# Performance work log

Hardware: AMD Instinct MI355X
Metric: run time of the kernel (lower is better)

Reference implementation:

```python
import jax, jax.numpy as jnp
import numpy as np

N = 100000      # nodes
E = 800000      # edges
IN = 256        # input feature dim
HID = 64        # hidden_channels (= per-head out_channels)
HEADS = 2       # num_heads
L = 2           # num_layers
C = 40          # class_num
ALPHA = 0.5
EPS = 1e-5


def setup_inputs() -> dict:
    key = jax.random.key(0)
    ks = jax.random.split(key, 14)
    s = 0.05
    inp = {
        "x": jax.random.normal(ks[0], (N, IN), dtype=jnp.float32),
        "edge_index": jax.random.randint(ks[1], (2, E), 0, N),
        "fc0_w": jax.random.normal(ks[2], (IN, HID), dtype=jnp.float32) * s,
        "fc0_b": jnp.zeros((HID,), jnp.float32),
        "ln_w": jnp.ones((L + 1, HID), jnp.float32),
        "ln_b": jnp.zeros((L + 1, HID), jnp.float32),
        "Wq": jax.random.normal(ks[3], (L, HID, HID * HEADS), dtype=jnp.float32) * s,
        "Wk": jax.random.normal(ks[4], (L, HID, HID * HEADS), dtype=jnp.float32) * s,
        "Wv": jax.random.normal(ks[5], (L, HID, HID * HEADS), dtype=jnp.float32) * s,
        "bq": jnp.zeros((L, HID * HEADS), jnp.float32),
        "bk": jnp.zeros((L, HID * HEADS), jnp.float32),
        "bv": jnp.zeros((L, HID * HEADS), jnp.float32),
        "fco_w": jax.random.normal(ks[6], (HID, C), dtype=jnp.float32) * s,
        "fco_b": jnp.zeros((C,), jnp.float32),
    }
    return inp


def _layernorm(x, w, b):
    mu = jnp.mean(x, axis=-1, keepdims=True)
    var = jnp.mean((x - mu) ** 2, axis=-1, keepdims=True)
    return (x - mu) * jax.lax.rsqrt(var + EPS) * w + b


def _simple_attn(q, k, v):
    # q,k: [N,H,M], v: [N,H,D]; kernelized (non-softmax) linear attention
    q = q / jnp.sqrt(jnp.sum(q * q))        # global L2 norm (torch.norm p=2)
    k = k / jnp.sqrt(jnp.sum(k * k))
    kvs = jnp.einsum('lhm,lhd->hmd', k, v)
    num = jnp.einsum('nhm,hmd->nhd', q, kvs) + jnp.sum(v, axis=0)  # [N,H,D]
    denom = jnp.einsum('nhm,hm->nh', q, jnp.sum(k, axis=0))[..., None]
    denom = denom + jnp.asarray(q.shape[0], q.dtype)
    return num / denom


def _gcn_conv(v, row, col):
    # v: [N,H,D]; out[n] = sum_{e: col[e]==n} w_e * v[row[e]]
    n = v.shape[0]
    deg = jax.ops.segment_sum(jnp.ones((row.shape[0],), v.dtype), col,
                              num_segments=n)
    val = jnp.sqrt(1.0 / deg[col]) * jnp.sqrt(1.0 / deg[row])
    val = jnp.nan_to_num(val, nan=0.0, posinf=0.0, neginf=0.0)
    v2 = v.reshape(n, -1)                    # [N, H*D]
    msg = val[:, None] * v2[row]             # [E, H*D]
    out = jax.ops.segment_sum(msg, col, num_segments=n)
    return out.reshape(v.shape)


def reference(x, edge_index, fc0_w, fc0_b, ln_w, ln_b, Wq, Wk, Wv, bq, bk, bv,
              fco_w, fco_b):
    row, col = edge_index[0], edge_index[1]
    h = x @ fc0_w + fc0_b
    h = _layernorm(h, ln_w[0], ln_b[0])
    h = jax.nn.relu(h)
    prev = h
    for i in range(L):
        q = (h @ Wq[i] + bq[i]).reshape(-1, HEADS, HID)
        k = (h @ Wk[i] + bk[i]).reshape(-1, HEADS, HID)
        v = (h @ Wv[i] + bv[i]).reshape(-1, HEADS, HID)
        out = _simple_attn(q, k, v) + _gcn_conv(v, row, col)
        out = out.mean(axis=1)               # mean over heads -> [N,HID]
        h = ALPHA * out + (1.0 - ALPHA) * prev
        h = _layernorm(h, ln_w[i + 1], ln_b[i + 1])
        prev = h
    return h @ fco_w + fco_b
```

## Files before the change

### kernel.cpp

```cpp
#include <hip/hip_runtime.h>
#include <math.h>

#define NNODES 100000
#define NEDGES 800000
#define DIN    256
#define HID    64
#define NC     40
#define NL     2
#define EPSL   1e-5f
#define CHUNK  1024
#define NCHUNK ((NNODES + CHUNK - 1) / CHUNK)
#define NB128  ((NNODES + 127) / 128)
#define NKVB   512
#define SLAB   8720

__device__ __forceinline__ float wave_allsum(float v) {
#pragma unroll
  for (int off = 32; off > 0; off >>= 1) v += __shfl_xor(v, off);
  return v;
}

__global__ void k_hist(const int* __restrict__ ei, int* __restrict__ deg) {
  for (int e = blockIdx.x * blockDim.x + threadIdx.x; e < NEDGES;
       e += gridDim.x * blockDim.x)
    atomicAdd(&deg[ei[NEDGES + e]], 1);
}

__global__ void k_scan1(const int* __restrict__ deg, int* __restrict__ csum) {
  __shared__ int sdata[256];
  int base = blockIdx.x * CHUNK;
  int s = 0;
  for (int t = threadIdx.x; t < CHUNK; t += 256) {
    int idx = base + t;
    if (idx < NNODES) s += deg[idx];
  }
  sdata[threadIdx.x] = s;
  __syncthreads();
  for (int off = 128; off > 0; off >>= 1) {
    if (threadIdx.x < off) sdata[threadIdx.x] += sdata[threadIdx.x + off];
    __syncthreads();
  }
  if (threadIdx.x == 0) csum[blockIdx.x] = sdata[0];
}

__global__ void k_scan2(const int* __restrict__ csum, int* __restrict__ cpref) {
  if (threadIdx.x == 0 && blockIdx.x == 0) {
    int run = 0;
    for (int i = 0; i < NCHUNK; ++i) { cpref[i] = run; run += csum[i]; }
  }
}

__global__ void k_scan3(const int* __restrict__ deg, const int* __restrict__ cpref,
                        int* __restrict__ offs) {
  __shared__ int bufA[CHUNK], bufB[CHUNK];
  int base = blockIdx.x * CHUNK;
  int orig[4];
#pragma unroll
  for (int i = 0; i < 4; ++i) {
    int t = threadIdx.x + i * 256;
    int idx = base + t;
    orig[i] = (idx < NNODES) ? deg[idx] : 0;
    bufA[t] = orig[i];
  }
  __syncthreads();
  int* src = bufA; int* dst = bufB;
  for (int off = 1; off < CHUNK; off <<= 1) {
#pragma unroll
    for (int i = 0; i < 4; ++i) {
      int t = threadIdx.x + i * 256;
      int vv = src[t];
      if (t >= off) vv += src[t - off];
      dst[t] = vv;
    }
    __syncthreads();
    int* tmp = src; src = dst; dst = tmp;
  }
  int cp = cpref[blockIdx.x];
#pragma unroll
  for (int i = 0; i < 4; ++i) {
    int t = threadIdx.x + i * 256;
    int idx = base + t;
    if (idx < NNODES) {
      offs[idx] = cp + src[t] - orig[i];
      if (idx == NNODES - 1) offs[NNODES] = cp + src[t];
    }
  }
}

__global__ void k_fill(const int* __restrict__ ei, const int* __restrict__ deg,
                       const int* __restrict__ offs, int* __restrict__ cursor,
                       int2* __restrict__ epack) {
  for (int e = blockIdx.x * blockDim.x + threadIdx.x; e < NEDGES;
       e += gridDim.x * blockDim.x) {
    int r = ei[e], c = ei[NEDGES + e];
    int pos = offs[c] + atomicAdd(&cursor[c], 1);
    int dc = deg[c], dr = deg[r];
    float w = (dr > 0)
        ? sqrtf(1.0f / (float)dc) * sqrtf(1.0f / (float)dr) : 0.0f;
    epack[pos] = make_int2(r, __float_as_int(w));
  }
}

__global__ __launch_bounds__(128) void k_fc0(
    const float* __restrict__ x, const float* __restrict__ w,
    const float* __restrict__ b, const float* __restrict__ lnw_,
    const float* __restrict__ lnb_, float* __restrict__ h) {
  __shared__ float xs[32 * 128];
  const int tid = threadIdx.x;
  const int base = blockIdx.x * 128;
  const int row = base + tid;
  const float4* x4 = (const float4*)x;
  float acc[64];
#pragma unroll
  for (int j = 0; j < 64; ++j) acc[j] = b[j];

  float4 pre[8];
#pragma unroll
  for (int i = 0; i < 8; ++i) {
    int r = i * 16 + (tid >> 3);
    int gr = base + r;
    pre[i] = (gr < NNODES) ? x4[(size_t)gr * 64 + (tid & 7)]
                           : make_float4(0.f, 0.f, 0.f, 0.f);
  }
  for (int c = 0; c < 8; ++c) {
    __syncthreads();
#pragma unroll
    for (int i = 0; i < 8; ++i) {
      int r = i * 16 + (tid >> 3);
      int kq = tid & 7;
      xs[(kq * 4 + 0) * 128 + r] = pre[i].x;
      xs[(kq * 4 + 1) * 128 + r] = pre[i].y;
      xs[(kq * 4 + 2) * 128 + r] = pre[i].z;
      xs[(kq * 4 + 3) * 128 + r] = pre[i].w;
    }
    __syncthreads();
    if (c < 7) {
#pragma unroll
      for (int i = 0; i < 8; ++i) {
        int r = i * 16 + (tid >> 3);
        int gr = base + r;
        pre[i] = (gr < NNODES) ? x4[(size_t)gr * 64 + (c + 1) * 8 + (tid & 7)]
                               : make_float4(0.f, 0.f, 0.f, 0.f);
      }
    }
    const float* wc = w + c * 32 * 64;
#pragma unroll 2
    for (int k = 0; k < 32; ++k) {
      float xv = xs[k * 128 + tid];
      const float* wr = wc + k * 64;
#pragma unroll
      for (int j = 0; j < 64; ++j) acc[j] = fmaf(xv, wr[j], acc[j]);
    }
  }
  if (row < NNODES) {
    float mu = 0.f;
#pragma unroll
    for (int j = 0; j < 64; ++j) mu += acc[j];
    mu *= (1.0f / 64.0f);
    float var = 0.f;
#pragma unroll
    for (int j = 0; j < 64; ++j) { float d = acc[j] - mu; var = fmaf(d, d, var); }
    float inv = 1.0f / sqrtf(var * (1.0f / 64.0f) + EPSL);
    float4* h4 = (float4*)(h + (size_t)row * 64);
#pragma unroll
    for (int jj = 0; jj < 16; ++jj) {
      float4 o;
      o.x = fmaxf((acc[4*jj+0] - mu) * inv * lnw_[4*jj+0] + lnb_[4*jj+0], 0.f);
      o.y = fmaxf((acc[4*jj+1] - mu) * inv * lnw_[4*jj+1] + lnb_[4*jj+1], 0.f);
      o.z = fmaxf((acc[4*jj+2] - mu) * inv * lnw_[4*jj+2] + lnb_[4*jj+2], 0.f);
      o.w = fmaxf((acc[4*jj+3] - mu) * inv * lnw_[4*jj+3] + lnb_[4*jj+3], 0.f);
      h4[jj] = o;
    }
  }
}

__global__ __launch_bounds__(128) void k_qkv(
    const float* __restrict__ h,
    const float* __restrict__ Wq, const float* __restrict__ Wk,
    const float* __restrict__ Wv,
    const float* __restrict__ bq, const float* __restrict__ bk,
    const float* __restrict__ bv,
    float* __restrict__ q, float* __restrict__ kk, float* __restrict__ vv,
    float* __restrict__ red) {
  __shared__ float hs[64 * 128];
  const int tid = threadIdx.x;
  const int base = blockIdx.x * 128;
  const int row = base + tid;
  const int mat = blockIdx.y;
  const float* W; const float* B; float* outp;
  if (mat == 0)      { W = Wq; B = bq; outp = q; }
  else if (mat == 1) { W = Wk; B = bk; outp = kk; }
  else               { W = Wv; B = bv; outp = vv; }

  const float4* h4 = (const float4*)h;
#pragma unroll
  for (int i = 0; i < 16; ++i) {
    int r = i * 8 + (tid >> 4);
    int kq = tid & 15;
    int gr = base + r;
    float4 t = (gr < NNODES) ? h4[(size_t)gr * 16 + kq]
                             : make_float4(0.f, 0.f, 0.f, 0.f);
    hs[(kq * 4 + 0) * 128 + r] = t.x;
    hs[(kq * 4 + 1) * 128 + r] = t.y;
    hs[(kq * 4 + 2) * 128 + r] = t.z;
    hs[(kq * 4 + 3) * 128 + r] = t.w;
  }
  __syncthreads();

  float sq = 0.f;
  for (int jc = 0; jc < 2; ++jc) {
    float acc[64];
#pragma unroll
    for (int j = 0; j < 64; ++j) acc[j] = B[jc * 64 + j];
#pragma unroll 2
    for (int k = 0; k < 64; ++k) {
      float xv = hs[k * 128 + tid];
      const float* wr = W + k * 128 + jc * 64;
#pragma unroll
      for (int j = 0; j < 64; ++j) acc[j] = fmaf(xv, wr[j], acc[j]);
    }
    if (row < NNODES) {
      float4* o4 = (float4*)(outp + (size_t)row * 128 + jc * 64);
#pragma unroll
      for (int jj = 0; jj < 16; ++jj)
        o4[jj] = make_float4(acc[4*jj], acc[4*jj+1], acc[4*jj+2], acc[4*jj+3]);
      if (mat == 0) {
#pragma unroll
        for (int j = 0; j < 64; ++j) sq = fmaf(acc[j], acc[j], sq);
      }
    }
  }
  if (mat == 0) {
    float t = wave_allsum(sq);
    if ((tid & 63) == 0) atomicAdd(&red[0], t);
  }
}

__global__ __launch_bounds__(256) void k_kvs(
    const float* __restrict__ k, const float* __restrict__ v,
    float* __restrict__ vh, float* __restrict__ slab) {
  __shared__ float kc[64 * 128], vc[64 * 128];
  __shared__ float sred[4];
  const int tid = threadIdx.x;
  const int hh = tid >> 7;
  const int t2 = tid & 127;
  const int mt = t2 >> 3;
  const int dt = t2 & 7;
  float acc[4][8];
#pragma unroll
  for (int a = 0; a < 4; ++a)
#pragma unroll
    for (int bq_ = 0; bq_ < 8; ++bq_) acc[a][bq_] = 0.f;
  float ksl = 0.f, vsl = 0.f, sqk = 0.f;
  const float4* k4 = (const float4*)k;
  const float4* v4 = (const float4*)v;

  for (int base = blockIdx.x * 64; base < NNODES; base += NKVB * 64) {
    if (base + 64 <= NNODES) {
      for (int t = tid; t < 2048; t += 256) {
        *(float4*)&kc[t * 4] = k4[(size_t)base * 32 + t];
        *(float4*)&vc[t * 4] = v4[(size_t)base * 32 + t];
      }
    } else {
      for (int t = tid; t < 2048; t += 256) {
        int node = base + (t >> 5);
        int c4 = t & 31;
        float4 kk4 = make_float4(0.f, 0.f, 0.f, 0.f), vv4 = kk4;
        if (node < NNODES) {
          kk4 = k4[(size_t)node * 32 + c4];
          vv4 = v4[(size_t)node * 32 + c4];
        }
        *(float4*)&kc[t * 4] = kk4;
        *(float4*)&vc[t * 4] = vv4;
      }
    }
    __syncthreads();
#pragma unroll 4
    for (int n = hh * 32; n < hh * 32 + 32; ++n) {
      float kv_ = kc[n * 128 + t2], vv_ = vc[n * 128 + t2];
      ksl += kv_; sqk = fmaf(kv_, kv_, sqk); vsl += vv_;
    }
    for (int t = tid; t < 4096; t += 256) {
      int n = t >> 6, d = t & 63;
      if (base + n < NNODES)
        vh[(size_t)(base + n) * 64 + d] =
            0.5f * (vc[n * 128 + d] + vc[n * 128 + 64 + d]);
    }
#pragma unroll 8
    for (int nn = 0; nn < 64; ++nn) {
      const float4 kk = *(const float4*)&kc[nn * 128 + hh * 64 + mt * 4];
      const float4 va = *(const float4*)&vc[nn * 128 + hh * 64 + dt * 8];
      const float4 vb = *(const float4*)&vc[nn * 128 + hh * 64 + dt * 8 + 4];
#pragma unroll
      for (int a = 0; a < 4; ++a) {
        float kx = (a == 0) ? kk.x : (a == 1) ? kk.y : (a == 2) ? kk.z : kk.w;
        acc[a][0] = fmaf(kx, va.x, acc[a][0]);
        acc[a][1] = fmaf(kx, va.y, acc[a][1]);
        acc[a][2] = fmaf(kx, va.z, acc[a][2]);
        acc[a][3] = fmaf(kx, va.w, acc[a][3]);
        acc[a][4] = fmaf(kx, vb.x, acc[a][4]);
        acc[a][5] = fmaf(kx, vb.y, acc[a][5]);
        acc[a][6] = fmaf(kx, vb.z, acc[a][6]);
        acc[a][7] = fmaf(kx, vb.w, acc[a][7]);
      }
    }
    __syncthreads();
  }
  float* sb = slab + (size_t)blockIdx.x * SLAB;
#pragma unroll
  for (int a = 0; a < 4; ++a) {
    *(float4*)&sb[hh * 4096 + (mt * 4 + a) * 64 + dt * 8] =
        make_float4(acc[a][0], acc[a][1], acc[a][2], acc[a][3]);
    *(float4*)&sb[hh * 4096 + (mt * 4 + a) * 64 + dt * 8 + 4] =
        make_float4(acc[a][4], acc[a][5], acc[a][6], acc[a][7]);
  }
  sb[8192 + tid] = ksl;
  sb[8448 + tid] = vsl;
  float ws = wave_allsum(sqk);
  if ((tid & 63) == 0) sred[tid >> 6] = ws;
  __syncthreads();
  if (tid == 0) sb[8704] = sred[0] + sred[1] + sred[2] + sred[3];
}

__global__ __launch_bounds__(256) void k_red(
    const float* __restrict__ slab, float* __restrict__ red) {
  int idx = blockIdx.x * 256 + threadIdx.x;
  if (idx < 8192) {
    float s = 0.f;
#pragma unroll 4
    for (int b = 0; b < NKVB; ++b) s += slab[(size_t)b * SLAB + idx];
    red[258 + idx] = s;
  } else if (idx < 8320) {
    int r = idx - 8192;
    float s = 0.f;
#pragma unroll 4
    for (int b = 0; b < NKVB; ++b)
      s += slab[(size_t)b * SLAB + 8192 + r] +
           slab[(size_t)b * SLAB + 8192 + 128 + r];
    red[2 + r] = s;
  } else if (idx < 8448) {
    int r = idx - 8320;
    float s = 0.f;
#pragma unroll 4
    for (int b = 0; b < NKVB; ++b)
      s += slab[(size_t)b * SLAB + 8448 + r] +
           slab[(size_t)b * SLAB + 8448 + 128 + r];
    red[130 + r] = s;
  } else if (idx == 8448) {
    float s = 0.f;
#pragma unroll 4
    for (int b = 0; b < NKVB; ++b) s += slab[(size_t)b * SLAB + 8704];
    red[1] = s;
  }
}

__global__ __launch_bounds__(128) void k_attn(
    const float* __restrict__ q, const float* __restrict__ red,
    float* __restrict__ attnm) {
  __shared__ float qs[64 * 128];
  const int tid = threadIdx.x;
  const int base = blockIdx.x * 128;
  const int row = base + tid;
  const float4* q4 = (const float4*)q;
  const float inv_qk = (1.0f / sqrtf(red[0])) * (1.0f / sqrtf(red[1]));
  float res[64];
  for (int hh = 0; hh < 2; ++hh) {
    if (hh) __syncthreads();
#pragma unroll
    for (int i = 0; i < 16; ++i) {
      int r = i * 8 + (tid >> 4);
      int kq = tid & 15;
      int gr = base + r;
      float4 t = (gr < NNODES) ? q4[(size_t)gr * 32 + hh * 16 + kq]
                               : make_float4(0.f, 0.f, 0.f, 0.f);
      qs[(kq * 4 + 0) * 128 + r] = t.x;
      qs[(kq * 4 + 1) * 128 + r] = t.y;
      qs[(kq * 4 + 2) * 128 + r] = t.z;
      qs[(kq * 4 + 3) * 128 + r] = t.w;
    }
    __syncthreads();
    float acc[64];
#pragma unroll
    for (int j = 0; j < 64; ++j) acc[j] = 0.f;
    float den = 0.f;
    const float* kvsb = red + 258 + hh * 4096;
    const float* ksb  = red + 2 + hh * 64;
#pragma unroll 2
    for (int m = 0; m < 64; ++m) {
      float qv = qs[m * 128 + tid];
      const float* kr = kvsb + m * 64;
#pragma unroll
      for (int j = 0; j < 64; ++j) acc[j] = fmaf(qv, kr[j], acc[j]);
      den = fmaf(qv, ksb[m], den);
    }
    float dd = 1.0f / (den * inv_qk + (float)NNODES);
    const float* vsb = red + 130 + hh * 64;
#pragma unroll
    for (int j = 0; j < 64; ++j) {
      float t = (acc[j] * inv_qk + vsb[j]) * dd;
      res[j] = (hh == 0) ? t : 0.5f * (res[j] + t);
    }
  }
  if (row < NNODES) {
    float4* o4 = (float4*)(attnm + (size_t)row * 64);
#pragma unroll
    for (int jj = 0; jj < 16; ++jj)
      o4[jj] = make_float4(res[4*jj], res[4*jj+1], res[4*jj+2], res[4*jj+3]);
  }
}

__global__ __launch_bounds__(256) void k_gcnln(
    const float* __restrict__ attnm, const float* __restrict__ vh,
    const float* __restrict__ prev, const int* __restrict__ offs,
    const int2* __restrict__ epack,
    const float* __restrict__ lnw_, const float* __restrict__ lnb_,
    float* __restrict__ hout) {
  const int wave = threadIdx.x >> 6, lane = threadIdx.x & 63;
  const float lw = lnw_[lane], lb = lnb_[lane];
  for (int node = blockIdx.x * 4 + wave; node < NNODES; node += gridDim.x * 4) {
    float g = 0.f;
    int s = offs[node], e = offs[node + 1];
    int i = s;
    for (; i + 1 < e; i += 2) {
      int2 e0 = epack[i], e1 = epack[i + 1];
      float v0 = vh[(size_t)e0.x * 64 + lane];
      float v1 = vh[(size_t)e1.x * 64 + lane];
      g = fmaf(__int_as_float(e0.y), v0, g);
      g = fmaf(__int_as_float(e1.y), v1, g);
    }
    if (i < e) {
      int2 e0 = epack[i];
      g = fmaf(__int_as_float(e0.y), vh[(size_t)e0.x * 64 + lane], g);
    }
    float om = attnm[(size_t)node * 64 + lane] + g;
    float pre = 0.5f * om + 0.5f * prev[(size_t)node * 64 + lane];
    float mu = wave_allsum(pre) * (1.0f / 64.0f);
    float d = pre - mu;
    float var = wave_allsum(d * d) * (1.0f / 64.0f);
    hout[(size_t)node * 64 + lane] = d * (1.0f / sqrtf(var + EPSL)) * lw + lb;
  }
}

__global__ __launch_bounds__(128) void k_final(
    const float* __restrict__ h, const float* __restrict__ w,
    const float* __restrict__ b, float* __restrict__ out) {
  __shared__ float hs[64 * 128];
  const int tid = threadIdx.x;
  const int base = blockIdx.x * 128;
  const int row = base + tid;
  const float4* h4 = (const float4*)h;
#pragma unroll
  for (int i = 0; i < 16; ++i) {
    int r = i * 8 + (tid >> 4);
    int kq = tid & 15;
    int gr = base + r;
    float4 t = (gr < NNODES) ? h4[(size_t)gr * 16 + kq]
                             : make_float4(0.f, 0.f, 0.f, 0.f);
    hs[(kq * 4 + 0) * 128 + r] = t.x;
    hs[(kq * 4 + 1) * 128 + r] = t.y;
    hs[(kq * 4 + 2) * 128 + r] = t.z;
    hs[(kq * 4 + 3) * 128 + r] = t.w;
  }
  __syncthreads();
  float acc[NC];
#pragma unroll
  for (int j = 0; j < NC; ++j) acc[j] = b[j];
#pragma unroll 2
  for (int k = 0; k < 64; ++k) {
    float xv = hs[k * 128 + tid];
    const float* wr = w + k * NC;
#pragma unroll
    for (int j = 0; j < NC; ++j) acc[j] = fmaf(xv, wr[j], acc[j]);
  }
  if (row < NNODES) {
    float4* o4 = (float4*)(out + (size_t)row * NC);
#pragma unroll
    for (int jj = 0; jj < NC / 4; ++jj)
      o4[jj] = make_float4(acc[4*jj], acc[4*jj+1], acc[4*jj+2], acc[4*jj+3]);
  }
}

extern "C" void kernel_launch(void* const* d_in, const int* in_sizes, int n_in,
                              void* d_out, int out_size, void* d_ws,
                              size_t ws_size, hipStream_t stream) {
  const float* x     = (const float*)d_in[0];
  const int*   ei    = (const int*)d_in[1];
  const float* fc0_w = (const float*)d_in[2];
  const float* fc0_b = (const float*)d_in[3];
  const float* ln_w  = (const float*)d_in[4];
  const float* ln_b  = (const float*)d_in[5];
  const float* Wq    = (const float*)d_in[6];
  const float* Wk    = (const float*)d_in[7];
  const float* Wv    = (const float*)d_in[8];
  const float* bq    = (const float*)d_in[9];
  const float* bk    = (const float*)d_in[10];
  const float* bv    = (const float*)d_in[11];
  const float* fco_w = (const float*)d_in[12];
  const float* fco_b = (const float*)d_in[13];
  float* out = (float*)d_out;

  char* p = (char*)d_ws;
  auto alloc = [&](size_t bytes) {
    char* r = p;
    p += (bytes + 255) & ~(size_t)255;
    return r;
  };
  float* q    = (float*)alloc(sizeof(float) * (size_t)NNODES * 128);
  float* kbuf = (float*)alloc(sizeof(float) * (size_t)NNODES * 128);
  float* vbuf = (float*)alloc(sizeof(float) * (size_t)NNODES * 128);
  float* hA   = (float*)alloc(sizeof(float) * (size_t)NNODES * HID);
  float* hB   = (float*)alloc(sizeof(float) * (size_t)NNODES * HID);
  float* vh   = (float*)alloc(sizeof(float) * (size_t)NNODES * HID);
  float* red  = (float*)alloc(sizeof(float) * 8704);
  float* slab = (float*)alloc(sizeof(float) * (size_t)NKVB * SLAB);
  int* deg    = (int*)alloc(sizeof(int) * NNODES);
  int* offs   = (int*)alloc(sizeof(int) * (NNODES + 1));
  int* cursor = (int*)alloc(sizeof(int) * NNODES);
  int2* epack = (int2*)alloc(sizeof(int2) * NEDGES);
  int* csum   = (int*)alloc(sizeof(int) * 128);
  int* cpref  = (int*)alloc(sizeof(int) * 128);
  float* attnm = kbuf;

  hipMemsetAsync(deg, 0, sizeof(int) * NNODES, stream);
  hipMemsetAsync(cursor, 0, sizeof(int) * NNODES, stream);
  k_hist<<<1024, 256, 0, stream>>>(ei, deg);
  k_scan1<<<NCHUNK, 256, 0, stream>>>(deg, csum);
  k_scan2<<<1, 64, 0, stream>>>(csum, cpref);
  k_scan3<<<NCHUNK, 256, 0, stream>>>(deg, cpref, offs);
  k_fill<<<1024, 256, 0, stream>>>(ei, deg, offs, cursor, epack);

  k_fc0<<<NB128, 128, 0, stream>>>(x, fc0_w, fc0_b, ln_w, ln_b, hA);

  float* hin = hA;
  float* hot = hB;
  for (int l = 0; l < NL; ++l) {
    hipMemsetAsync(red, 0, sizeof(float) * 2, stream);
    k_qkv<<<dim3(NB128, 3), 128, 0, stream>>>(hin,
        Wq + (size_t)l * HID * 128, Wk + (size_t)l * HID * 128,
        Wv + (size_t)l * HID * 128,
        bq + (size_t)l * 128, bk + (size_t)l * 128, bv + (size_t)l * 128,
        q, kbuf, vbuf, red);
    k_kvs<<<NKVB, 256, 0, stream>>>(kbuf, vbuf, vh, slab);
    k_red<<<34, 256, 0, stream>>>(slab, red);
    k_attn<<<NB128, 128, 0, stream>>>(q, red, attnm);
    k_gcnln<<<2048, 256, 0, stream>>>(attnm, vh, hin, offs, epack,
        ln_w + (size_t)(l + 1) * HID, ln_b + (size_t)(l + 1) * HID, hot);
    float* tmp = hin; hin = hot; hot = tmp;
  }

  k_final<<<NB128, 128, 0, stream>>>(hin, fco_w, fco_b, out);
}
```

Baseline: 1.165 ms.

## Hold weights in registers and stage weights in LDS across dense GEMM kernels

Restructures k_qkv so each wave owns one of Q/K/V and keeps its weight columns in registers while streaming rows from shared memory, replacing the 3-way grid split that reloaded h per matrix. k_attn likewise keeps the kvs matrices in registers per lane and computes the denominator via wave reductions, using 64-row blocks. k_fc0 and k_final stage weight tiles in LDS with padded strides to avoid scalar/global weight loads and bank conflicts, and k_fc0 drops its register prefetch of x. The cost is higher register pressure (128 weight floats per lane) and the loss of prefetch overlap in fc0.

```diff
diff --git a/kernel.cpp b/kernel.cpp
--- a/kernel.cpp
+++ b/kernel.cpp
@@ -11,6 +11,7 @@
 #define CHUNK  1024
 #define NCHUNK ((NNODES + CHUNK - 1) / CHUNK)
 #define NB128  ((NNODES + 127) / 128)
+#define NB64   ((NNODES + 63) / 64)
 #define NKVB   512
 #define SLAB   8720
 
@@ -105,7 +106,8 @@
     const float* __restrict__ x, const float* __restrict__ w,
     const float* __restrict__ b, const float* __restrict__ lnw_,
     const float* __restrict__ lnb_, float* __restrict__ h) {
-  __shared__ float xs[32 * 128];
+  __shared__ float xs[32 * 132];
+  __shared__ float ws[32 * 64];
   const int tid = threadIdx.x;
   const int base = blockIdx.x * 128;
   const int row = base + tid;
@@ -114,40 +116,31 @@
 #pragma unroll
   for (int j = 0; j < 64; ++j) acc[j] = b[j];
 
-  float4 pre[8];
-#pragma unroll
-  for (int i = 0; i < 8; ++i) {
-    int r = i * 16 + (tid >> 3);
-    int gr = base + r;
-    pre[i] = (gr < NNODES) ? x4[(size_t)gr * 64 + (tid & 7)]
-                           : make_float4(0.f, 0.f, 0.f, 0.f);
-  }
   for (int c = 0; c < 8; ++c) {
     __syncthreads();
 #pragma unroll
     for (int i = 0; i < 8; ++i) {
       int r = i * 16 + (tid >> 3);
       int kq = tid & 7;
-      xs[(kq * 4 + 0) * 128 + r] = pre[i].x;
-      xs[(kq * 4 + 1) * 128 + r] = pre[i].y;
-      xs[(kq * 4 + 2) * 128 + r] = pre[i].z;
-      xs[(kq * 4 + 3) * 128 + r] = pre[i].w;
+      int gr = base + r;
+      float4 t = (gr < NNODES) ? x4[(size_t)gr * 64 + c * 8 + kq]
+                               : make_float4(0.f, 0.f, 0.f, 0.f);
+      xs[(kq * 4 + 0) * 132 + r] = t.x;
+      xs[(kq * 4 + 1) * 132 + r] = t.y;
+      xs[(kq * 4 + 2) * 132 + r] = t.z;
+      xs[(kq * 4 + 3) * 132 + r] = t.w;
+    }
+    {
+      const float4* w4 = (const float4*)(w + c * 32 * 64);
+      float4* s4 = (float4*)ws;
+#pragma unroll
+      for (int t = 0; t < 4; ++t) s4[tid + t * 128] = w4[tid + t * 128];
     }
     __syncthreads();
-    if (c < 7) {
-#pragma unroll
-      for (int i = 0; i < 8; ++i) {
-        int r = i * 16 + (tid >> 3);
-        int gr = base + r;
-        pre[i] = (gr < NNODES) ? x4[(size_t)gr * 64 + (c + 1) * 8 + (tid & 7)]
-                               : make_float4(0.f, 0.f, 0.f, 0.f);
-      }
-    }
-    const float* wc = w + c * 32 * 64;
 #pragma unroll 2
     for (int k = 0; k < 32; ++k) {
-      float xv = xs[k * 128 + tid];
-      const float* wr = wc + k * 64;
+      float xv = xs[k * 132 + tid];
+      const float* wr = &ws[k * 64];
 #pragma unroll
       for (int j = 0; j < 64; ++j) acc[j] = fmaf(xv, wr[j], acc[j]);
     }
@@ -174,7 +167,7 @@
   }
 }
 
-__global__ __launch_bounds__(128) void k_qkv(
+__global__ __launch_bounds__(192, 3) void k_qkv(
     const float* __restrict__ h,
     const float* __restrict__ Wq, const float* __restrict__ Wk,
     const float* __restrict__ Wv,
@@ -182,57 +175,61 @@
     const float* __restrict__ bv,
     float* __restrict__ q, float* __restrict__ kk, float* __restrict__ vv,
     float* __restrict__ red) {
-  __shared__ float hs[64 * 128];
+  __shared__ float hs[128 * 64];
   const int tid = threadIdx.x;
+  const int wave = tid / 64;
+  const int lane = tid & 63;
   const int base = blockIdx.x * 128;
-  const int row = base + tid;
-  const int mat = blockIdx.y;
-  const float* W; const float* B; float* outp;
-  if (mat == 0)      { W = Wq; B = bq; outp = q; }
-  else if (mat == 1) { W = Wk; B = bk; outp = kk; }
-  else               { W = Wv; B = bv; outp = vv; }
-
-  const float4* h4 = (const float4*)h;
-#pragma unroll
-  for (int i = 0; i < 16; ++i) {
-    int r = i * 8 + (tid >> 4);
-    int kq = tid & 15;
-    int gr = base + r;
-    float4 t = (gr < NNODES) ? h4[(size_t)gr * 16 + kq]
-                             : make_float4(0.f, 0.f, 0.f, 0.f);
-    hs[(kq * 4 + 0) * 128 + r] = t.x;
-    hs[(kq * 4 + 1) * 128 + r] = t.y;
-    hs[(kq * 4 + 2) * 128 + r] = t.z;
-    hs[(kq * 4 + 3) * 128 + r] = t.w;
-  }
-  __syncthreads();
-
+  const int nrow = NNODES - base;
+  {
+    const float4* h4 = (const float4*)(h + (size_t)base * 64);
+    float4* s4 = (float4*)hs;
+    for (int t = tid; t < 2048; t += 192) {
+      float4 val = make_float4(0.f, 0.f, 0.f, 0.f);
+      if ((t >> 4) < nrow) val = h4[t];
+      s4[t] = val;
+    }
+  }
+  const float* W = (wave == 0) ? Wq : (wave == 1) ? Wk : Wv;
+  const float* B = (wave == 0) ? bq : (wave == 1) ? bk : bv;
+  float* outp    = (wave == 0) ? q  : (wave == 1) ? kk : vv;
+  const int j0 = lane * 2;
+  float w0[64], w1[64];
+#pragma unroll
+  for (int t = 0; t < 64; ++t) {
+    float2 wv_ = *(const float2*)(W + t * 128 + j0);
+    w0[t] = wv_.x; w1[t] = wv_.y;
+  }
+  const float b0 = B[j0], b1 = B[j0 + 1];
+  __syncthreads();
   float sq = 0.f;
-  for (int jc = 0; jc < 2; ++jc) {
-    float acc[64];
-#pragma unroll
-    for (int j = 0; j < 64; ++j) acc[j] = B[jc * 64 + j];
-#pragma unroll 2
-    for (int k = 0; k < 64; ++k) {
-      float xv = hs[k * 128 + tid];
-      const float* wr = W + k * 128 + jc * 64;
-#pragma unroll
-      for (int j = 0; j < 64; ++j) acc[j] = fmaf(xv, wr[j], acc[j]);
-    }
-    if (row < NNODES) {
-      float4* o4 = (float4*)(outp + (size_t)row * 128 + jc * 64);
-#pragma unroll
-      for (int jj = 0; jj < 16; ++jj)
-        o4[jj] = make_float4(acc[4*jj], acc[4*jj+1], acc[4*jj+2], acc[4*jj+3]);
-      if (mat == 0) {
-#pragma unroll
-        for (int j = 0; j < 64; ++j) sq = fmaf(acc[j], acc[j], sq);
-      }
-    }
-  }
-  if (mat == 0) {
+  for (int r = 0; r < 128; r += 2) {
+    float a0 = b0, a1 = b1, c0 = b0, c1 = b1;
+#pragma unroll
+    for (int t = 0; t < 16; ++t) {
+      float4 ha = *(const float4*)&hs[r * 64 + t * 4];
+      float4 hb = *(const float4*)&hs[(r + 1) * 64 + t * 4];
+      a0 = fmaf(ha.x, w0[4*t+0], a0); a1 = fmaf(ha.x, w1[4*t+0], a1);
+      a0 = fmaf(ha.y, w0[4*t+1], a0); a1 = fmaf(ha.y, w1[4*t+1], a1);
+      a0 = fmaf(ha.z, w0[4*t+2], a0); a1 = fmaf(ha.z, w1[4*t+2], a1);
+      a0 = fmaf(ha.w, w0[4*t+3], a0); a1 = fmaf(ha.w, w1[4*t+3], a1);
+      c0 = fmaf(hb.x, w0[4*t+0], c0); c1 = fmaf(hb.x, w1[4*t+0], c1);
+      c0 = fmaf(hb.y, w0[4*t+1], c0); c1 = fmaf(hb.y, w1[4*t+1], c1);
+      c0 = fmaf(hb.z, w0[4*t+2], c0); c1 = fmaf(hb.z, w1[4*t+2], c1);
+      c0 = fmaf(hb.w, w0[4*t+3], c0); c1 = fmaf(hb.w, w1[4*t+3], c1);
+    }
+    if (r < nrow) {
+      *(float2*)(outp + (size_t)(base + r) * 128 + j0) = make_float2(a0, a1);
+      if (wave == 0) { sq = fmaf(a0, a0, sq); sq = fmaf(a1, a1, sq); }
+    }
+    if (r + 1 < nrow) {
+      *(float2*)(outp + (size_t)(base + r + 1) * 128 + j0) = make_float2(c0, c1);
+      if (wave == 0) { sq = fmaf(c0, c0, sq); sq = fmaf(c1, c1, sq); }
+    }
+  }
+  if (wave == 0) {
     float t = wave_allsum(sq);
-    if ((tid & 63) == 0) atomicAdd(&red[0], t);
+    if (lane == 0) atomicAdd(&red[0], t);
   }
 }
 
@@ -354,58 +351,69 @@
   }
 }
 
-__global__ __launch_bounds__(128) void k_attn(
+__global__ __launch_bounds__(128, 3) void k_attn(
     const float* __restrict__ q, const float* __restrict__ red,
     float* __restrict__ attnm) {
   __shared__ float qs[64 * 128];
   const int tid = threadIdx.x;
-  const int base = blockIdx.x * 128;
-  const int row = base + tid;
-  const float4* q4 = (const float4*)q;
+  const int lane = tid & 63;
+  const int wave = tid >> 6;
+  const int base = blockIdx.x * 64;
+  const int nrow = NNODES - base;
+  {
+    const float4* r4 = (const float4*)(red + 258);
+    float4* s4 = (float4*)qs;
+    for (int t = tid; t < 2048; t += 128) s4[t] = r4[t];
+  }
+  __syncthreads();
+  float kvA[64], kvB[64];
+#pragma unroll
+  for (int m = 0; m < 64; ++m) {
+    kvA[m] = qs[m * 64 + lane];
+    kvB[m] = qs[4096 + m * 64 + lane];
+  }
+  const float ksA = red[2 + lane],   ksB = red[2 + 64 + lane];
+  const float vsA = red[130 + lane], vsB = red[130 + 64 + lane];
   const float inv_qk = (1.0f / sqrtf(red[0])) * (1.0f / sqrtf(red[1]));
-  float res[64];
-  for (int hh = 0; hh < 2; ++hh) {
-    if (hh) __syncthreads();
-#pragma unroll
-    for (int i = 0; i < 16; ++i) {
-      int r = i * 8 + (tid >> 4);
-      int kq = tid & 15;
-      int gr = base + r;
-      float4 t = (gr < NNODES) ? q4[(size_t)gr * 32 + hh * 16 + kq]
-                               : make_float4(0.f, 0.f, 0.f, 0.f);
-      qs[(kq * 4 + 0) * 128 + r] = t.x;
-      qs[(kq * 4 + 1) * 128 + r] = t.y;
-      qs[(kq * 4 + 2) * 128 + r] = t.z;
-      qs[(kq * 4 + 3) * 128 + r] = t.w;
-    }
-    __syncthreads();
-    float acc[64];
-#pragma unroll
-    for (int j = 0; j < 64; ++j) acc[j] = 0.f;
-    float den = 0.f;
-    const float* kvsb = red + 258 + hh * 4096;
-    const float* ksb  = red + 2 + hh * 64;
-#pragma unroll 2
-    for (int m = 0; m < 64; ++m) {
-      float qv = qs[m * 128 + tid];
-      const float* kr = kvsb + m * 64;
-#pragma unroll
-      for (int j = 0; j < 64; ++j) acc[j] = fmaf(qv, kr[j], acc[j]);
-      den = fmaf(qv, ksb[m], den);
-    }
-    float dd = 1.0f / (den * inv_qk + (float)NNODES);
-    const float* vsb = red + 130 + hh * 64;
-#pragma unroll
-    for (int j = 0; j < 64; ++j) {
-      float t = (acc[j] * inv_qk + vsb[j]) * dd;
-      res[j] = (hh == 0) ? t : 0.5f * (res[j] + t);
-    }
-  }
-  if (row < NNODES) {
-    float4* o4 = (float4*)(attnm + (size_t)row * 64);
-#pragma unroll
-    for (int jj = 0; jj < 16; ++jj)
-      o4[jj] = make_float4(res[4*jj], res[4*jj+1], res[4*jj+2], res[4*jj+3]);
+  __syncthreads();
+  {
+    const float4* q4 = (const float4*)(q + (size_t)base * 128);
+    float4* s4 = (float4*)qs;
+    for (int t = tid; t < 2048; t += 128) {
+      float4 val = make_float4(0.f, 0.f, 0.f, 0.f);
+      if ((t >> 5) < nrow) val = q4[t];
+      s4[t] = val;
+    }
+  }
+  __syncthreads();
+  const int r0 = wave * 32;
+  for (int r = r0; r < r0 + 32; r += 2) {
+    float a0 = 0.f, a1 = 0.f, c0 = 0.f, c1 = 0.f;
+#pragma unroll
+    for (int t = 0; t < 16; ++t) {
+      float4 qa = *(const float4*)&qs[r * 128 + t * 4];
+      float4 qb = *(const float4*)&qs[r * 128 + 64 + t * 4];
+      float4 ra = *(const float4*)&qs[(r + 1) * 128 + t * 4];
+      float4 rb = *(const float4*)&qs[(r + 1) * 128 + 64 + t * 4];
+      a0 = fmaf(qa.x, kvA[4*t+0], a0); a1 = fmaf(qb.x, kvB[4*t+0], a1);
+      a0 = fmaf(qa.y, kvA[4*t+1], a0); a1 = fmaf(qb.y, kvB[4*t+1], a1);
+      a0 = fmaf(qa.z, kvA[4*t+2], a0); a1 = fmaf(qb.z, kvB[4*t+2], a1);
+      a0 = fmaf(qa.w, kvA[4*t+3], a0); a1 = fmaf(qb.w, kvB[4*t+3], a1);
+      c0 = fmaf(ra.x, kvA[4*t+0], c0); c1 = fmaf(rb.x, kvB[4*t+0], c1);
+      c0 = fmaf(ra.y, kvA[4*t+1], c0); c1 = fmaf(rb.y, kvB[4*t+1], c1);
+      c0 = fmaf(ra.z, kvA[4*t+2], c0); c1 = fmaf(rb.z, kvB[4*t+2], c1);
+      c0 = fmaf(ra.w, kvA[4*t+3], c0); c1 = fmaf(rb.w, kvB[4*t+3], c1);
+    }
+    float d0a = wave_allsum(qs[r * 128 + lane] * ksA);
+    float d1a = wave_allsum(qs[r * 128 + 64 + lane] * ksB);
+    float d0b = wave_allsum(qs[(r + 1) * 128 + lane] * ksA);
+    float d1b = wave_allsum(qs[(r + 1) * 128 + 64 + lane] * ksB);
+    float t0 = (a0 * inv_qk + vsA) / (d0a * inv_qk + (float)NNODES);
+    float t1 = (a1 * inv_qk + vsB) / (d1a * inv_qk + (float)NNODES);
+    float u0 = (c0 * inv_qk + vsA) / (d0b * inv_qk + (float)NNODES);
+    float u1 = (c1 * inv_qk + vsB) / (d1b * inv_qk + (float)NNODES);
+    if (r < nrow)     attnm[(size_t)(base + r) * 64 + lane] = 0.5f * (t0 + t1);
+    if (r + 1 < nrow) attnm[(size_t)(base + r + 1) * 64 + lane] = 0.5f * (u0 + u1);
   }
 }
 
@@ -444,10 +452,16 @@
 __global__ __launch_bounds__(128) void k_final(
     const float* __restrict__ h, const float* __restrict__ w,
     const float* __restrict__ b, float* __restrict__ out) {
-  __shared__ float hs[64 * 128];
+  __shared__ float hs[64 * 132];
+  __shared__ float wl[HID * NC];
   const int tid = threadIdx.x;
   const int base = blockIdx.x * 128;
   const int row = base + tid;
+  {
+    const float4* w4 = (const float4*)w;
+    float4* s4 = (float4*)wl;
+    for (int t = tid; t < 640; t += 128) s4[t] = w4[t];
+  }
   const float4* h4 = (const float4*)h;
 #pragma unroll
   for (int i = 0; i < 16; ++i) {
@@ -456,10 +470,10 @@
     int gr = base + r;
     float4 t = (gr < NNODES) ? h4[(size_t)gr * 16 + kq]
                              : make_float4(0.f, 0.f, 0.f, 0.f);
-    hs[(kq * 4 + 0) * 128 + r] = t.x;
-    hs[(kq * 4 + 1) * 128 + r] = t.y;
-    hs[(kq * 4 + 2) * 128 + r] = t.z;
-    hs[(kq * 4 + 3) * 128 + r] = t.w;
+    hs[(kq * 4 + 0) * 132 + r] = t.x;
+    hs[(kq * 4 + 1) * 132 + r] = t.y;
+    hs[(kq * 4 + 2) * 132 + r] = t.z;
+    hs[(kq * 4 + 3) * 132 + r] = t.w;
   }
   __syncthreads();
   float acc[NC];
@@ -467,8 +481,8 @@
   for (int j = 0; j < NC; ++j) acc[j] = b[j];
 #pragma unroll 2
   for (int k = 0; k < 64; ++k) {
-    float xv = hs[k * 128 + tid];
-    const float* wr = w + k * NC;
+    float xv = hs[k * 132 + tid];
+    const float* wr = &wl[k * NC];
 #pragma unroll
     for (int j = 0; j < NC; ++j) acc[j] = fmaf(xv, wr[j], acc[j]);
   }
@@ -535,14 +549,14 @@
   float* hot = hB;
   for (int l = 0; l < NL; ++l) {
     hipMemsetAsync(red, 0, sizeof(float) * 2, stream);
-    k_qkv<<<dim3(NB128, 3), 128, 0, stream>>>(hin,
+    k_qkv<<<NB128, 192, 0, stream>>>(hin,
         Wq + (size_t)l * HID * 128, Wk + (size_t)l * HID * 128,
         Wv + (size_t)l * HID * 128,
         bq + (size_t)l * 128, bk + (size_t)l * 128, bv + (size_t)l * 128,
         q, kbuf, vbuf, red);
     k_kvs<<<NKVB, 256, 0, stream>>>(kbuf, vbuf, vh, slab);
     k_red<<<34, 256, 0, stream>>>(slab, red);
-    k_attn<<<NB128, 128, 0, stream>>>(q, red, attnm);
+    k_attn<<<NB64, 128, 0, stream>>>(q, red, attnm);
     k_gcnln<<<2048, 256, 0, stream>>>(attnm, vh, hin, offs, epack,
         ln_w + (size_t)(l + 1) * HID, ln_b + (size_t)(l + 1) * HID, hot);
     float* tmp = hin; hin = hot; hot = tmp;
```

After: 4.500 ms. 286% more time.
